# Optimization experiments

Hardware: AMD Instinct MI355X
Metric: run time of the kernel (lower is better)

## Reference

```python
import jax, jax.numpy as jnp
import numpy as np

B, T, E = 2, 2048, 1024
H = 16
D = E // H  # head_dim = 64


def setup_inputs() -> dict:
    key = jax.random.key(0)
    k1, k2, k3 = jax.random.split(key, 3)
    x = jax.random.normal(k1, (B, T, E), dtype=jnp.float32)
    w_qkv = jax.random.normal(k2, (3 * E, E), dtype=jnp.float32) * 0.02
    w_proj = jax.random.normal(k3, (E, E), dtype=jnp.float32) * 0.02
    return {"x": x, "w_qkv": w_qkv, "w_proj": w_proj}


def reference(x, w_qkv, w_proj):
    b, t, c = x.shape
    # qkv projection (torch Linear: x @ W^T), split into q,k,v
    qkv = jnp.einsum('btc,fc->btf', x, w_qkv)  # [B,T,3E]
    q, k, v = jnp.split(qkv, 3, axis=-1)
    # [B,T,E] -> [B,H,T,D]
    q = q.reshape(b, t, H, D).transpose(0, 2, 1, 3)
    k = k.reshape(b, t, H, D).transpose(0, 2, 1, 3)
    v = v.reshape(b, t, H, D).transpose(0, 2, 1, 3)
    scale = 1.0 / jnp.sqrt(jnp.float32(D))
    att = jnp.einsum('bhqd,bhkd->bhqk', q, k) * scale  # [B,H,T,T]
    causal = jnp.tril(jnp.ones((t, t), dtype=bool))
    att = jnp.where(causal[None, None], att, -jnp.inf)
    att = jax.nn.softmax(att, axis=-1)
    out = jnp.einsum('bhqk,bhkd->bhqd', att, v)  # [B,H,T,D]
    out = out.transpose(0, 2, 1, 3).reshape(b, t, c)  # [B,T,E]
    out = jnp.einsum('btc,oc->bto', out, w_proj)
    return out
```

## Files before the change

### kernel.cpp

```cpp
#include <hip/hip_runtime.h>
#include <stdint.h>
#include <stddef.h>

typedef __attribute__((ext_vector_type(8))) short s16x8;
typedef __attribute__((ext_vector_type(4))) short s16x4;
typedef __attribute__((ext_vector_type(4))) float f32x4;

#define B_  2
#define T_  2048
#define E_  1024
#define H_  16
#define E3_ 3072

__device__ __forceinline__ short f2bf(float f) {
  union { float f; uint32_t u; } v; v.f = f;
  uint32_t u = v.u;
  return (short)((u + 0x7FFFu + ((u >> 16) & 1u)) >> 16);
}

__device__ __forceinline__ uint32_t fbits(float f) {
  union { float f; uint32_t u; } v; v.f = f; return v.u;
}

__device__ __forceinline__ void gload_lds16(const short* g, short* l) {
  __builtin_amdgcn_global_load_lds(
      (__attribute__((address_space(1))) void*)(const_cast<short*>(g)),
      (__attribute__((address_space(3))) void*)(l), 16, 0, 0);
}

__global__ void castk_all(const float* __restrict__ x, const float* __restrict__ wqkv,
                          const float* __restrict__ wproj, short* __restrict__ xb,
                          short* __restrict__ wqkvb, short* __restrict__ wprojb) {
  const int bid = blockIdx.x;
  const float* in; short* out; int i; float sc = 1.0f;
  if (bid < 4096)      { in = x;     out = xb;     i = bid * 256 + threadIdx.x; }
  else if (bid < 7168) { in = wqkv;  out = wqkvb;  i = (bid - 4096) * 256 + threadIdx.x;
                         if (i < 262144) sc = 0.18033688011112042f; }
  else                 { in = wproj; out = wprojb; i = (bid - 7168) * 256 + threadIdx.x; }
  const float4 v = ((const float4*)in)[i];
  s16x4 o;
  o[0] = f2bf(v.x * sc); o[1] = f2bf(v.y * sc);
  o[2] = f2bf(v.z * sc); o[3] = f2bf(v.w * sc);
  ((s16x4*)out)[i] = o;
}

template <int OUT_BF16>
__global__ void gemm_nt_128(const short* __restrict__ A, const short* __restrict__ B,
                            void* __restrict__ Cv, int M, int N, int K) {
  __shared__ short As[128 * 32];
  __shared__ short Bs[128 * 32];
  const int tid  = threadIdx.x;
  const int lane = tid & 63;
  const int w    = tid >> 6;
  const int quad = lane >> 4;
  const int l16  = lane & 15;
  const int wm   = (w >> 1) * 64;
  const int wn   = (w & 1) * 64;
  const int bm   = blockIdx.y * 128;
  const int bn   = blockIdx.x * 128;

  f32x4 acc[4][4];
#pragma unroll
  for (int i = 0; i < 4; i++)
#pragma unroll
    for (int j = 0; j < 4; j++) acc[i][j] = (f32x4){0.f, 0.f, 0.f, 0.f};

  const int srow = w * 32 + (lane >> 2);
  const int scol = (lane & 3) * 8;
  const short* gA = A + (size_t)(bm + srow) * K + scol;
  const short* gB = B + (size_t)(bn + srow) * K + scol;
  short* lA = As + (w * 32) * 32;
  short* lB = Bs + (w * 32) * 32;

  for (int k0 = 0; k0 < K; k0 += 32) {
    __syncthreads();
    gload_lds16(gA + k0,          lA);
    gload_lds16(gA + 16 * K + k0, lA + 16 * 32);
    gload_lds16(gB + k0,          lB);
    gload_lds16(gB + 16 * K + k0, lB + 16 * 32);
    __syncthreads();

    s16x8 a[4], b[4];
#pragma unroll
    for (int i = 0; i < 4; i++)
      a[i] = *(const s16x8*)&As[(wm + i * 16 + l16) * 32 + quad * 8];
#pragma unroll
    for (int j = 0; j < 4; j++)
      b[j] = *(const s16x8*)&Bs[(wn + j * 16 + l16) * 32 + quad * 8];
#pragma unroll
    for (int i = 0; i < 4; i++)
#pragma unroll
      for (int j = 0; j < 4; j++)
        acc[i][j] = __builtin_amdgcn_mfma_f32_16x16x32_bf16(a[i], b[j], acc[i][j], 0, 0, 0);
  }

#pragma unroll
  for (int i = 0; i < 4; i++) {
    const int row0 = bm + wm + i * 16 + quad * 4;
#pragma unroll
    for (int j = 0; j < 4; j++) {
      const int col = bn + wn + j * 16 + l16;
#pragma unroll
      for (int r = 0; r < 4; r++) {
        const size_t idx = (size_t)(row0 + r) * N + col;
        if (OUT_BF16) ((short*)Cv)[idx] = f2bf(acc[i][j][r]);
        else          ((float*)Cv)[idx] = acc[i][j][r];
      }
    }
  }
}

__global__ void vtrans(const short* __restrict__ qkv, short* __restrict__ vt) {
  __shared__ __align__(16) short tile[64 * 68];
  const int tt = blockIdx.x;
  const int bh = blockIdx.y;
  const int b = bh >> 4, h = bh & 15;
  const int tid = threadIdx.x;
#pragma unroll
  for (int k = 0; k < 4; k++) {
    const int c = tid + k * 256;
    const int r = c >> 4;
    const int c4 = (c & 15) * 4;
    s16x4 v = *(const s16x4*)(qkv + (size_t)(b * T_ + tt * 64 + r) * E3_ + 2 * E_ + h * 64 + c4);
    *(s16x4*)&tile[r * 68 + c4] = v;
  }
  __syncthreads();
#pragma unroll
  for (int k = 0; k < 4; k++) {
    const int c = tid + k * 256;
    const int d = c >> 4;
    const int t4 = (c & 15) * 4;
    s16x4 v;
    v[0] = tile[(t4 + 0) * 68 + d];
    v[1] = tile[(t4 + 1) * 68 + d];
    v[2] = tile[(t4 + 2) * 68 + d];
    v[3] = tile[(t4 + 3) * 68 + d];
    *(s16x4*)(vt + (size_t)(bh * 64 + d) * T_ + tt * 64 + t4) = v;
  }
}

__global__ void __launch_bounds__(256, 4)
attn_kernel(const short* __restrict__ qkv, const short* __restrict__ vt,
            short* __restrict__ attout) {
  __shared__ short Ks[2][64 * 64];
  __shared__ short Vs[2][64 * 64];
  __shared__ short Ps[4][16 * 64];
  __shared__ float Ls[4][16];
  const int tid  = threadIdx.x;
  const int lane = tid & 63;
  const int w    = tid >> 6;
  const int quad = lane >> 4;
  const int l16  = lane & 15;
  const int bh = blockIdx.x;
  const int b = bh >> 4, h = bh & 15;
  const int qt  = (int)(gridDim.y - 1) - (int)blockIdx.y;
  const int q0b = qt * 64;
  const int q0w = q0b + w * 16;
  const float NEG_INF = -__builtin_inff();

  const short* qbase = qkv + (size_t)(b * T_ + q0w + l16) * E3_ + h * 64 + quad * 8;
  const s16x8 qf0 = *(const s16x8*)(qbase);
  const s16x8 qf1 = *(const s16x8*)(qbase + 32);

  const int srl = lane >> 3;
  const int sgc = ((lane & 7) ^ srl) * 8;
  const short* gK = qkv + (size_t)(b * T_) * E3_ + E_ + h * 64 + sgc;
  const short* gV = vt + (size_t)(bh * 64) * T_ + sgc;

  f32x4 o[4];
#pragma unroll
  for (int j = 0; j < 4; j++) o[j] = (f32x4){0.f, 0.f, 0.f, 0.f};
  float lsum = 0.f;
  const int swz = (l16 & 7);

#pragma unroll
  for (int i = 0; i < 2; i++) {
    const int row = w * 16 + i * 8 + srl;
    gload_lds16(gK + (size_t)row * E3_, &Ks[0][(w * 16 + i * 8) * 64]);
    gload_lds16(gV + (size_t)row * T_,  &Vs[0][(w * 16 + i * 8) * 64]);
  }
  __syncthreads();

  for (int kv0 = 0; kv0 <= q0b; kv0 += 64) {
    const int cur = (kv0 >> 6) & 1;

    s16x8 kf[2][4];
#pragma unroll
    for (int c = 0; c < 2; c++)
#pragma unroll
      for (int j = 0; j < 4; j++)
        kf[c][j] = *(const s16x8*)&Ks[cur][(j * 16 + l16) * 64 + (((c * 4 + quad) ^ swz) * 8)];

    if (kv0 + 64 <= q0b) {
#pragma unroll
      for (int i = 0; i < 2; i++) {
        const int row = w * 16 + i * 8 + srl;
        gload_lds16(gK + (size_t)(kv0 + 64 + row) * E3_, &Ks[cur ^ 1][(w * 16 + i * 8) * 64]);
        gload_lds16(gV + (size_t)row * T_ + kv0 + 64,    &Vs[cur ^ 1][(w * 16 + i * 8) * 64]);
      }
    }

    f32x4 s[4];
#pragma unroll
    for (int j = 0; j < 4; j++) s[j] = (f32x4){0.f, 0.f, 0.f, 0.f};
#pragma unroll
    for (int c = 0; c < 2; c++)
#pragma unroll
      for (int j = 0; j < 4; j++)
        s[j] = __builtin_amdgcn_mfma_f32_16x16x32_bf16(kf[c][j], c == 0 ? qf0 : qf1, s[j], 0, 0, 0);

    if (kv0 == q0b) {
#pragma unroll
      for (int j = 0; j < 4; j++)
#pragma unroll
        for (int r = 0; r < 4; r++)
          if (j * 16 + quad * 4 + r > w * 16 + l16) s[j][r] = NEG_INF;
    }

#pragma unroll
    for (int j = 0; j < 4; j++) {
      const float p0 = exp2f(s[j][0]);
      const float p1 = exp2f(s[j][1]);
      const float p2 = exp2f(s[j][2]);
      const float p3 = exp2f(s[j][3]);
      lsum += (p0 + p1) + (p2 + p3);
      int2 pk;
      pk.x = (int)((fbits(p0) >> 16) | (fbits(p1) & 0xFFFF0000u));
      pk.y = (int)((fbits(p2) >> 16) | (fbits(p3) & 0xFFFF0000u));
      short* pw = &Ps[w][l16 * 64 + (((2 * j + (quad >> 1)) ^ swz) * 8) + (quad & 1) * 4];
      *(int2*)pw = pk;
    }
    __asm volatile("s_waitcnt lgkmcnt(0)" ::: "memory");

#pragma unroll
    for (int c = 0; c < 2; c++) {
      const s16x8 pf = *(const s16x8*)&Ps[w][l16 * 64 + (((4 * c + quad) ^ swz) * 8)];
#pragma unroll
      for (int j = 0; j < 4; j++) {
        const s16x8 vf = *(const s16x8*)&Vs[cur][(j * 16 + l16) * 64 + (((c * 4 + quad) ^ swz) * 8)];
        o[j] = __builtin_amdgcn_mfma_f32_16x16x32_bf16(pf, vf, o[j], 0, 0, 0);
      }
    }

    __syncthreads();
  }

  lsum += __shfl_xor(lsum, 16);
  lsum += __shfl_xor(lsum, 32);
  Ls[w][l16] = lsum;
  __asm volatile("s_waitcnt lgkmcnt(0)" ::: "memory");

#pragma unroll
  for (int r = 0; r < 4; r++) {
    const float inv = 1.0f / Ls[w][quad * 4 + r];
    const int q = q0w + quad * 4 + r;
    short* ob = attout + ((size_t)(b * T_ + q) * H_ + h) * 64 + l16;
    ob[0]  = f2bf(o[0][r] * inv);
    ob[16] = f2bf(o[1][r] * inv);
    ob[32] = f2bf(o[2][r] * inv);
    ob[48] = f2bf(o[3][r] * inv);
  }
}

extern "C" void kernel_launch(void* const* d_in, const int* in_sizes, int n_in,
                              void* d_out, int out_size, void* d_ws, size_t ws_size,
                              hipStream_t stream) {
  const float* x     = (const float*)d_in[0];
  const float* wqkv  = (const float*)d_in[1];
  const float* wproj = (const float*)d_in[2];

  if (ws_size < 58720256u) return;
  short* ws     = (short*)d_ws;
  short* xb     = ws;
  short* wqkvb  = xb + 4194304;
  short* wprojb = wqkvb + 3145728;
  short* qkv    = wprojb + 1048576;
  short* vt     = qkv + 12582912;
  short* attb   = vt + 4194304;

  castk_all<<<8192, 256, 0, stream>>>(x, wqkv, wproj, xb, wqkvb, wprojb);
  gemm_nt_128<1><<<dim3(24, 32), 256, 0, stream>>>(xb, wqkvb, qkv, 4096, 3072, 1024);
  vtrans<<<dim3(32, 32), 256, 0, stream>>>(qkv, vt);
  attn_kernel<<<dim3(32, 32), 256, 0, stream>>>(qkv, vt, attb);
  gemm_nt_128<0><<<dim3(8, 32), 256, 0, stream>>>(attb, wprojb, d_out, 4096, 1024, 1024);
}
```

Before: 183.1 us.

## Fuse V transpose into QKV GEMM epilogue and pair causal query tiles per block

The QKV GEMM now writes the V third of its output straight into the transposed vt layout, so the separate vtrans kernel and its launch go away. The attention grid is halved: each block handles query tile pr and then 31-pr, balancing causal work across blocks and prefetching the next phase's first KV tile. Row sums are now computed by an MFMA against a ones vector instead of scalar adds and shuffles, P packing uses a byte-permute instruction, and launch bounds drop to 2 blocks per CU. The risks are scattered 8-byte vt stores in the GEMM epilogue, and fewer but longer blocks reducing parallelism slack.

```diff
diff --git a/kernel.cpp b/kernel.cpp
--- a/kernel.cpp
+++ b/kernel.cpp
@@ -44,9 +44,10 @@
   ((s16x4*)out)[i] = o;
 }
 
-template <int OUT_BF16>
+template <int MODE>
 __global__ void gemm_nt_128(const short* __restrict__ A, const short* __restrict__ B,
-                            void* __restrict__ Cv, int M, int N, int K) {
+                            void* __restrict__ Cv, short* __restrict__ vt,
+                            int M, int N, int K) {
   __shared__ short As[128 * 32];
   __shared__ short Bs[128 * 32];
   const int tid  = threadIdx.x;
@@ -94,58 +95,44 @@
         acc[i][j] = __builtin_amdgcn_mfma_f32_16x16x32_bf16(a[i], b[j], acc[i][j], 0, 0, 0);
   }
 
-#pragma unroll
-  for (int i = 0; i < 4; i++) {
-    const int row0 = bm + wm + i * 16 + quad * 4;
-#pragma unroll
-    for (int j = 0; j < 4; j++) {
-      const int col = bn + wn + j * 16 + l16;
-#pragma unroll
-      for (int r = 0; r < 4; r++) {
-        const size_t idx = (size_t)(row0 + r) * N + col;
-        if (OUT_BF16) ((short*)Cv)[idx] = f2bf(acc[i][j][r]);
-        else          ((float*)Cv)[idx] = acc[i][j][r];
+  if (MODE == 2 && bn >= 2 * E_) {
+#pragma unroll
+    for (int i = 0; i < 4; i++) {
+      const int token = bm + wm + i * 16 + quad * 4;
+      const int bb = token >> 11, t = token & (T_ - 1);
+#pragma unroll
+      for (int j = 0; j < 4; j++) {
+        const int col = bn + wn + j * 16 + l16 - 2 * E_;
+        s16x4 pk;
+#pragma unroll
+        for (int r = 0; r < 4; r++) pk[r] = f2bf(acc[i][j][r]);
+        *(s16x4*)&vt[((size_t)(bb * H_ + (col >> 6)) * 64 + (col & 63)) * T_ + t] = pk;
+      }
+    }
+  } else {
+#pragma unroll
+    for (int i = 0; i < 4; i++) {
+      const int row0 = bm + wm + i * 16 + quad * 4;
+#pragma unroll
+      for (int j = 0; j < 4; j++) {
+        const int col = bn + wn + j * 16 + l16;
+#pragma unroll
+        for (int r = 0; r < 4; r++) {
+          const size_t idx = (size_t)(row0 + r) * N + col;
+          if (MODE == 2) ((short*)Cv)[idx] = f2bf(acc[i][j][r]);
+          else           ((float*)Cv)[idx] = acc[i][j][r];
+        }
       }
     }
   }
 }
 
-__global__ void vtrans(const short* __restrict__ qkv, short* __restrict__ vt) {
-  __shared__ __align__(16) short tile[64 * 68];
-  const int tt = blockIdx.x;
-  const int bh = blockIdx.y;
-  const int b = bh >> 4, h = bh & 15;
-  const int tid = threadIdx.x;
-#pragma unroll
-  for (int k = 0; k < 4; k++) {
-    const int c = tid + k * 256;
-    const int r = c >> 4;
-    const int c4 = (c & 15) * 4;
-    s16x4 v = *(const s16x4*)(qkv + (size_t)(b * T_ + tt * 64 + r) * E3_ + 2 * E_ + h * 64 + c4);
-    *(s16x4*)&tile[r * 68 + c4] = v;
-  }
-  __syncthreads();
-#pragma unroll
-  for (int k = 0; k < 4; k++) {
-    const int c = tid + k * 256;
-    const int d = c >> 4;
-    const int t4 = (c & 15) * 4;
-    s16x4 v;
-    v[0] = tile[(t4 + 0) * 68 + d];
-    v[1] = tile[(t4 + 1) * 68 + d];
-    v[2] = tile[(t4 + 2) * 68 + d];
-    v[3] = tile[(t4 + 3) * 68 + d];
-    *(s16x4*)(vt + (size_t)(bh * 64 + d) * T_ + tt * 64 + t4) = v;
-  }
-}
-
-__global__ void __launch_bounds__(256, 4)
+__global__ void __launch_bounds__(256, 2)
 attn_kernel(const short* __restrict__ qkv, const short* __restrict__ vt,
             short* __restrict__ attout) {
   __shared__ short Ks[2][64 * 64];
   __shared__ short Vs[2][64 * 64];
   __shared__ short Ps[4][16 * 64];
-  __shared__ float Ls[4][16];
   const int tid  = threadIdx.x;
   const int lane = tid & 63;
   const int w    = tid >> 6;
@@ -153,112 +140,114 @@
   const int l16  = lane & 15;
   const int bh = blockIdx.x;
   const int b = bh >> 4, h = bh & 15;
-  const int qt  = (int)(gridDim.y - 1) - (int)blockIdx.y;
-  const int q0b = qt * 64;
-  const int q0w = q0b + w * 16;
+  const int pr = blockIdx.y;
   const float NEG_INF = -__builtin_inff();
-
-  const short* qbase = qkv + (size_t)(b * T_ + q0w + l16) * E3_ + h * 64 + quad * 8;
-  const s16x8 qf0 = *(const s16x8*)(qbase);
-  const s16x8 qf1 = *(const s16x8*)(qbase + 32);
 
   const int srl = lane >> 3;
   const int sgc = ((lane & 7) ^ srl) * 8;
   const short* gK = qkv + (size_t)(b * T_) * E3_ + E_ + h * 64 + sgc;
   const short* gV = vt + (size_t)(bh * 64) * T_ + sgc;
-
-  f32x4 o[4];
-#pragma unroll
-  for (int j = 0; j < 4; j++) o[j] = (f32x4){0.f, 0.f, 0.f, 0.f};
-  float lsum = 0.f;
   const int swz = (l16 & 7);
 
-#pragma unroll
-  for (int i = 0; i < 2; i++) {
-    const int row = w * 16 + i * 8 + srl;
-    gload_lds16(gK + (size_t)row * E3_, &Ks[0][(w * 16 + i * 8) * 64]);
-    gload_lds16(gV + (size_t)row * T_,  &Vs[0][(w * 16 + i * 8) * 64]);
-  }
+  s16x8 ones;
+#pragma unroll
+  for (int i = 0; i < 8; i++) ones[i] = (short)0x3F80;
+
+  auto stage = [&](int kv0s, int bf) {
+#pragma unroll
+    for (int i = 0; i < 2; i++) {
+      const int row = w * 16 + i * 8 + srl;
+      gload_lds16(gK + (size_t)(kv0s + row) * E3_, &Ks[bf][(w * 16 + i * 8) * 64]);
+      gload_lds16(gV + (size_t)row * T_ + kv0s,    &Vs[bf][(w * 16 + i * 8) * 64]);
+    }
+  };
+
+  stage(0, 0);
   __syncthreads();
 
-  for (int kv0 = 0; kv0 <= q0b; kv0 += 64) {
-    const int cur = (kv0 >> 6) & 1;
-
-    s16x8 kf[2][4];
-#pragma unroll
-    for (int c = 0; c < 2; c++)
-#pragma unroll
-      for (int j = 0; j < 4; j++)
-        kf[c][j] = *(const s16x8*)&Ks[cur][(j * 16 + l16) * 64 + (((c * 4 + quad) ^ swz) * 8)];
-
-    if (kv0 + 64 <= q0b) {
-#pragma unroll
-      for (int i = 0; i < 2; i++) {
-        const int row = w * 16 + i * 8 + srl;
-        gload_lds16(gK + (size_t)(kv0 + 64 + row) * E3_, &Ks[cur ^ 1][(w * 16 + i * 8) * 64]);
-        gload_lds16(gV + (size_t)row * T_ + kv0 + 64,    &Vs[cur ^ 1][(w * 16 + i * 8) * 64]);
-      }
-    }
-
-    f32x4 s[4];
-#pragma unroll
-    for (int j = 0; j < 4; j++) s[j] = (f32x4){0.f, 0.f, 0.f, 0.f};
-#pragma unroll
-    for (int c = 0; c < 2; c++)
-#pragma unroll
-      for (int j = 0; j < 4; j++)
-        s[j] = __builtin_amdgcn_mfma_f32_16x16x32_bf16(kf[c][j], c == 0 ? qf0 : qf1, s[j], 0, 0, 0);
-
-    if (kv0 == q0b) {
-#pragma unroll
-      for (int j = 0; j < 4; j++)
-#pragma unroll
-        for (int r = 0; r < 4; r++)
-          if (j * 16 + quad * 4 + r > w * 16 + l16) s[j][r] = NEG_INF;
-    }
-
-#pragma unroll
-    for (int j = 0; j < 4; j++) {
-      const float p0 = exp2f(s[j][0]);
-      const float p1 = exp2f(s[j][1]);
-      const float p2 = exp2f(s[j][2]);
-      const float p3 = exp2f(s[j][3]);
-      lsum += (p0 + p1) + (p2 + p3);
-      int2 pk;
-      pk.x = (int)((fbits(p0) >> 16) | (fbits(p1) & 0xFFFF0000u));
-      pk.y = (int)((fbits(p2) >> 16) | (fbits(p3) & 0xFFFF0000u));
-      short* pw = &Ps[w][l16 * 64 + (((2 * j + (quad >> 1)) ^ swz) * 8) + (quad & 1) * 4];
-      *(int2*)pw = pk;
-    }
-    __asm volatile("s_waitcnt lgkmcnt(0)" ::: "memory");
-
-#pragma unroll
-    for (int c = 0; c < 2; c++) {
-      const s16x8 pf = *(const s16x8*)&Ps[w][l16 * 64 + (((4 * c + quad) ^ swz) * 8)];
+  int g = 0;
+#pragma unroll 1
+  for (int ph = 0; ph < 2; ph++) {
+    const int qt  = ph ? (31 - pr) : pr;
+    const int q0b = qt * 64;
+    const int q0w = q0b + w * 16;
+
+    const short* qbase = qkv + (size_t)(b * T_ + q0w + l16) * E3_ + h * 64 + quad * 8;
+    const s16x8 qf0 = *(const s16x8*)(qbase);
+    const s16x8 qf1 = *(const s16x8*)(qbase + 32);
+
+    f32x4 o[4]; f32x4 ol = (f32x4){0.f, 0.f, 0.f, 0.f};
+#pragma unroll
+    for (int j = 0; j < 4; j++) o[j] = (f32x4){0.f, 0.f, 0.f, 0.f};
+
+    for (int kv0 = 0; kv0 <= q0b; kv0 += 64, g++) {
+      const int cur = g & 1;
+
+      s16x8 kf[2][4];
+#pragma unroll
+      for (int c = 0; c < 2; c++)
+#pragma unroll
+        for (int j = 0; j < 4; j++)
+          kf[c][j] = *(const s16x8*)&Ks[cur][(j * 16 + l16) * 64 + (((c * 4 + quad) ^ swz) * 8)];
+
+      if (kv0 + 64 <= q0b) stage(kv0 + 64, cur ^ 1);
+      else if (ph == 0)    stage(0, cur ^ 1);
+
+      f32x4 s[4];
+#pragma unroll
+      for (int j = 0; j < 4; j++) s[j] = (f32x4){0.f, 0.f, 0.f, 0.f};
+#pragma unroll
+      for (int c = 0; c < 2; c++)
+#pragma unroll
+        for (int j = 0; j < 4; j++)
+          s[j] = __builtin_amdgcn_mfma_f32_16x16x32_bf16(kf[c][j], c == 0 ? qf0 : qf1, s[j], 0, 0, 0);
+
+      if (kv0 == q0b) {
+#pragma unroll
+        for (int j = 0; j < 4; j++)
+#pragma unroll
+          for (int r = 0; r < 4; r++)
+            if (j * 16 + quad * 4 + r > w * 16 + l16) s[j][r] = NEG_INF;
+      }
+
 #pragma unroll
       for (int j = 0; j < 4; j++) {
-        const s16x8 vf = *(const s16x8*)&Vs[cur][(j * 16 + l16) * 64 + (((c * 4 + quad) ^ swz) * 8)];
-        o[j] = __builtin_amdgcn_mfma_f32_16x16x32_bf16(pf, vf, o[j], 0, 0, 0);
-      }
-    }
-
-    __syncthreads();
-  }
-
-  lsum += __shfl_xor(lsum, 16);
-  lsum += __shfl_xor(lsum, 32);
-  Ls[w][l16] = lsum;
-  __asm volatile("s_waitcnt lgkmcnt(0)" ::: "memory");
-
-#pragma unroll
-  for (int r = 0; r < 4; r++) {
-    const float inv = 1.0f / Ls[w][quad * 4 + r];
-    const int q = q0w + quad * 4 + r;
-    short* ob = attout + ((size_t)(b * T_ + q) * H_ + h) * 64 + l16;
-    ob[0]  = f2bf(o[0][r] * inv);
-    ob[16] = f2bf(o[1][r] * inv);
-    ob[32] = f2bf(o[2][r] * inv);
-    ob[48] = f2bf(o[3][r] * inv);
+        const float p0 = exp2f(s[j][0]);
+        const float p1 = exp2f(s[j][1]);
+        const float p2 = exp2f(s[j][2]);
+        const float p3 = exp2f(s[j][3]);
+        int2 pk;
+        pk.x = (int)__builtin_amdgcn_perm(fbits(p1), fbits(p0), 0x07060302u);
+        pk.y = (int)__builtin_amdgcn_perm(fbits(p3), fbits(p2), 0x07060302u);
+        short* pw = &Ps[w][l16 * 64 + (((2 * j + (quad >> 1)) ^ swz) * 8) + (quad & 1) * 4];
+        *(int2*)pw = pk;
+      }
+      __asm volatile("s_waitcnt lgkmcnt(0)" ::: "memory");
+
+#pragma unroll
+      for (int c = 0; c < 2; c++) {
+        const s16x8 pf = *(const s16x8*)&Ps[w][l16 * 64 + (((4 * c + quad) ^ swz) * 8)];
+        ol = __builtin_amdgcn_mfma_f32_16x16x32_bf16(pf, ones, ol, 0, 0, 0);
+#pragma unroll
+        for (int j = 0; j < 4; j++) {
+          const s16x8 vf = *(const s16x8*)&Vs[cur][(j * 16 + l16) * 64 + (((c * 4 + quad) ^ swz) * 8)];
+          o[j] = __builtin_amdgcn_mfma_f32_16x16x32_bf16(pf, vf, o[j], 0, 0, 0);
+        }
+      }
+
+      __syncthreads();
+    }
+
+#pragma unroll
+    for (int r = 0; r < 4; r++) {
+      const float inv = 1.0f / ol[r];
+      const int q = q0w + quad * 4 + r;
+      short* ob = attout + ((size_t)(b * T_ + q) * H_ + h) * 64 + l16;
+      ob[0]  = f2bf(o[0][r] * inv);
+      ob[16] = f2bf(o[1][r] * inv);
+      ob[32] = f2bf(o[2][r] * inv);
+      ob[48] = f2bf(o[3][r] * inv);
+    }
   }
 }
 
@@ -279,8 +268,7 @@
   short* attb   = vt + 4194304;
 
   castk_all<<<8192, 256, 0, stream>>>(x, wqkv, wproj, xb, wqkvb, wprojb);
-  gemm_nt_128<1><<<dim3(24, 32), 256, 0, stream>>>(xb, wqkvb, qkv, 4096, 3072, 1024);
-  vtrans<<<dim3(32, 32), 256, 0, stream>>>(qkv, vt);
-  attn_kernel<<<dim3(32, 32), 256, 0, stream>>>(qkv, vt, attb);
-  gemm_nt_128<0><<<dim3(8, 32), 256, 0, stream>>>(attb, wprojb, d_out, 4096, 1024, 1024);
-}
+  gemm_nt_128<2><<<dim3(24, 32), 256, 0, stream>>>(xb, wqkvb, qkv, vt, 4096, 3072, 1024);
+  attn_kernel<<<dim3(32, 16), 256, 0, stream>>>(qkv, vt, attb);
+  gemm_nt_128<0><<<dim3(8, 32), 256, 0, stream>>>(attb, wprojb, d_out, nullptr, 4096, 1024, 1024);
+}
```

After: 175.8 us. -4.0%, faster.
